# Optimization experiments

Hardware: AMD Instinct MI355X
Metric: run time of the kernel (lower is better)

## Reference

```python
import jax, jax.numpy as jnp
import numpy as np
import math

B, S, D, DFF = 32, 2048, 512, 512


def setup_inputs() -> dict:
    key = jax.random.key(0)
    ks = jax.random.split(key, 10)
    s = 1.0 / math.sqrt(D)
    inp = {
        "x": jax.random.normal(ks[0], (B, S, D), dtype=jnp.float32),
        "Wq": jax.random.uniform(ks[1], (DFF, D), jnp.float32, -s, s),
        "bq": jax.random.uniform(ks[2], (DFF,), jnp.float32, -s, s),
        "Wk": jax.random.uniform(ks[3], (DFF, D), jnp.float32, -s, s),
        "bk": jax.random.uniform(ks[4], (DFF,), jnp.float32, -s, s),
        "Wv": jax.random.uniform(ks[5], (DFF, D), jnp.float32, -s, s),
        "bv": jax.random.uniform(ks[6], (DFF,), jnp.float32, -s, s),
        "Wt": jax.random.uniform(ks[7], (1, S), jnp.float32, -1.0 / math.sqrt(S), 1.0 / math.sqrt(S)),
        "bt": jax.random.uniform(ks[8], (1,), jnp.float32, -1.0 / math.sqrt(S), 1.0 / math.sqrt(S)),
    }
    return inp


def reference(x, Wq, bq, Wk, bk, Wv, bv, Wt, bt):
    # QKV projections: [B,S,DFF]
    q = jnp.einsum('bsd,fd->bsf', x, Wq) + bq
    k = jnp.einsum('bsd,fd->bsf', x, Wk) + bk
    v = jnp.einsum('bsd,fd->bsf', x, Wv) + bv
    # attention scores: [B,S,S]
    scores = jnp.einsum('bsf,btf->bst', q, k) / math.sqrt(DFF)
    # temporal reduction Linear(S->1): [B,S,1] -> [B,S]
    ta = jnp.einsum('bst,t->bs', scores, Wt[0]) + bt[0]
    # V-weighted sum: [B,DFF]
    latent = jnp.einsum('bsf,bs->bf', v, ta)
    return latent
```

## Files before the change

### kernel.cpp

```cpp
#include <hip/hip_runtime.h>

#define NB 32
#define NS 2048
#define ND 512
#define NFF 512
#define SCALE 0.044194173824159216f

__device__ __forceinline__ float dot4(float4 a, float4 b) {
    return a.x * b.x + a.y * b.y + a.z * b.z + a.w * b.w;
}

__device__ __forceinline__ float wave_reduce(float p) {
#pragma unroll
    for (int m = 1; m < 64; m <<= 1) p += __shfl_xor(p, m, 64);
    return p;
}

__global__ void __launch_bounds__(256) k_xw(const float* __restrict__ x,
                                            const float* __restrict__ Wt,
                                            float* __restrict__ xwp) {
    const int b = blockIdx.x >> 5;
    const int chunk = blockIdx.x & 31;
    const int s0 = chunk * 64;
    const int t = threadIdx.x;
    const int col = t & 127;
    const int half = t >> 7;
    const float4* xb = (const float4*)(x + (size_t)b * NS * ND);
    float4 acc = make_float4(0.f, 0.f, 0.f, 0.f);
#pragma unroll 4
    for (int i = 0; i < 32; i++) {
        int s = s0 + half + 2 * i;
        float w = Wt[s];
        float4 v = xb[(size_t)s * 128 + col];
        acc.x += w * v.x; acc.y += w * v.y; acc.z += w * v.z; acc.w += w * v.w;
    }
    __shared__ float4 red[128];
    if (half == 1) red[col] = acc;
    __syncthreads();
    if (half == 0) {
        float4 o = red[col];
        o.x += acc.x; o.y += acc.y; o.z += acc.z; o.w += acc.w;
        ((float4*)xwp)[(size_t)blockIdx.x * 128 + col] = o;
    }
}

__global__ void __launch_bounds__(1024) k_kwq(const float* __restrict__ xwp,
                                              const float* __restrict__ Wt,
                                              const float* __restrict__ Wk,
                                              const float* __restrict__ bk,
                                              const float* __restrict__ Wq,
                                              const float* __restrict__ bq,
                                              const float* __restrict__ bt,
                                              float* __restrict__ wqs,
                                              float* __restrict__ cb2) {
    const int b = blockIdx.x;
    const int t = threadIdx.x;
    const int wv = t >> 6;
    const int lane = t & 63;
    __shared__ float xw[ND];
    __shared__ float kwl[NFF];
    __shared__ float part[2][ND];
    __shared__ float cbred[16];
    __shared__ float swt_s;

    if (t < ND) {
        float a = 0.f;
        const float* p = xwp + (size_t)b * 32 * ND + t;
#pragma unroll
        for (int c = 0; c < 32; c++) a += p[c * ND];
        xw[t] = a;
    }
    if (wv == 15) {
        float a = 0.f;
#pragma unroll
        for (int j = 0; j < 32; j++) a += Wt[j * 64 + lane];
        a = wave_reduce(a);
        if (lane == 0) swt_s = a;
    }
    __syncthreads();

    {
        const float4* xw4 = (const float4*)xw;
        const float4 xa = xw4[lane];
        const float4 xc = xw4[64 + lane];
        const float sw = swt_s;
        float cbp = 0.f;
#pragma unroll 4
        for (int j = 0; j < 32; j++) {
            int f = wv * 32 + j;
            const float4* wr = (const float4*)(Wk + (size_t)f * ND);
            float p = dot4(xa, wr[lane]) + dot4(xc, wr[64 + lane]);
            p = wave_reduce(p);
            if (lane == 0) {
                float kf = p + bk[f] * sw;
                kwl[f] = kf;
                cbp += kf * bq[f];
            }
        }
        if (lane == 0) cbred[wv] = cbp;
    }
    __syncthreads();

    {
        const int d = t & 511;
        const int h = t >> 9;
        float acc = 0.f;
        const int f0 = h * 256;
#pragma unroll 8
        for (int j = 0; j < 256; j++) {
            int f = f0 + j;
            acc += kwl[f] * Wq[(size_t)f * ND + d];
        }
        part[h][d] = acc;
        if (t == 0) {
            float s = 0.f;
#pragma unroll
            for (int w = 0; w < 16; w++) s += cbred[w];
            cb2[b] = SCALE * s + bt[0];
        }
    }
    __syncthreads();
    if (t < ND) wqs[b * ND + t] = SCALE * (part[0][t] + part[1][t]);
}

__global__ void __launch_bounds__(256) k_ta_xt(const float* __restrict__ x,
                                               const float* __restrict__ wqs,
                                               const float* __restrict__ cb2,
                                               float* __restrict__ xtp,
                                               float* __restrict__ stp) {
    const int b = blockIdx.x >> 5;
    const int chunk = blockIdx.x & 31;
    const int wave = threadIdx.x >> 6;
    const int lane = threadIdx.x & 63;
    const float4* xb = (const float4*)(x + (size_t)b * NS * ND);
    const float4* wq4 = (const float4*)(wqs + b * ND);
    const float4 w0 = wq4[lane];
    const float4 w1 = wq4[64 + lane];
    const float c = cb2[b];
    float4 a0 = make_float4(0.f, 0.f, 0.f, 0.f);
    float4 a1 = make_float4(0.f, 0.f, 0.f, 0.f);
    float sta = 0.f;
#pragma unroll 2
    for (int i = 0; i < 16; i++) {
        int s = chunk * 64 + wave * 16 + i;
        float4 v0 = xb[(size_t)s * 128 + lane];
        float4 v1 = xb[(size_t)s * 128 + 64 + lane];
        float p = dot4(v0, w0) + dot4(v1, w1);
        p = wave_reduce(p);
        float ta = p + c;
        a0.x += ta * v0.x; a0.y += ta * v0.y; a0.z += ta * v0.z; a0.w += ta * v0.w;
        a1.x += ta * v1.x; a1.y += ta * v1.y; a1.z += ta * v1.z; a1.w += ta * v1.w;
        sta += ta;
    }
    __shared__ float4 sh0[4][64];
    __shared__ float4 sh1[4][64];
    __shared__ float stw[4];
    sh0[wave][lane] = a0;
    sh1[wave][lane] = a1;
    if (lane == 0) stw[wave] = sta;
    __syncthreads();
    const int t = threadIdx.x;
    float4* dst = (float4*)xtp + (size_t)blockIdx.x * 128;
    if (t < 64) {
        float4 s0 = sh0[0][t], s1 = sh0[1][t], s2 = sh0[2][t], s3 = sh0[3][t];
        dst[t] = make_float4(s0.x + s1.x + s2.x + s3.x,
                             s0.y + s1.y + s2.y + s3.y,
                             s0.z + s1.z + s2.z + s3.z,
                             s0.w + s1.w + s2.w + s3.w);
    } else if (t < 128) {
        int l = t - 64;
        float4 s0 = sh1[0][l], s1 = sh1[1][l], s2 = sh1[2][l], s3 = sh1[3][l];
        dst[64 + l] = make_float4(s0.x + s1.x + s2.x + s3.x,
                                  s0.y + s1.y + s2.y + s3.y,
                                  s0.z + s1.z + s2.z + s3.z,
                                  s0.w + s1.w + s2.w + s3.w);
    } else if (t == 128) {
        stp[blockIdx.x] = stw[0] + stw[1] + stw[2] + stw[3];
    }
}

__global__ void __launch_bounds__(256) k_latent(const float* __restrict__ xtp,
                                                const float* __restrict__ stp,
                                                const float* __restrict__ Wv,
                                                const float* __restrict__ bv,
                                                float* __restrict__ out) {
    const int b = blockIdx.x >> 3;
    const int t = threadIdx.x;
    __shared__ float xt[ND];
    __shared__ float sts;
    {
        float a0 = 0.f, a1 = 0.f;
        const float* p = xtp + (size_t)b * 32 * ND;
#pragma unroll
        for (int c = 0; c < 32; c++) {
            a0 += p[c * ND + t];
            a1 += p[c * ND + 256 + t];
        }
        xt[t] = a0;
        xt[256 + t] = a1;
        if (t == 0) {
            float s = 0.f;
            const float* sp = stp + b * 32;
#pragma unroll
            for (int c = 0; c < 32; c++) s += sp[c];
            sts = s;
        }
    }
    __syncthreads();
    const int wv = t >> 6;
    const int lane = t & 63;
    const int f0 = ((blockIdx.x & 7) * 4 + wv) * 16;
    const float4* xt4 = (const float4*)xt;
    const float4 xa = xt4[lane];
    const float4 xc = xt4[64 + lane];
    const float stb = sts;
#pragma unroll 4
    for (int j = 0; j < 16; j++) {
        int f = f0 + j;
        const float4* wr = (const float4*)(Wv + (size_t)f * ND);
        float p = dot4(xa, wr[lane]) + dot4(xc, wr[64 + lane]);
        p = wave_reduce(p);
        if (lane == 0) out[b * NFF + f] = p + bv[f] * stb;
    }
}

extern "C" void kernel_launch(void* const* d_in, const int* in_sizes, int n_in,
                              void* d_out, int out_size, void* d_ws, size_t ws_size,
                              hipStream_t stream) {
    const float* x  = (const float*)d_in[0];
    const float* Wq = (const float*)d_in[1];
    const float* bq = (const float*)d_in[2];
    const float* Wk = (const float*)d_in[3];
    const float* bk = (const float*)d_in[4];
    const float* Wv = (const float*)d_in[5];
    const float* bv = (const float*)d_in[6];
    const float* Wt = (const float*)d_in[7];
    const float* bt = (const float*)d_in[8];
    float* out = (float*)d_out;

    float* w = (float*)d_ws;
    float* xwp = w;
    float* xtp = w + 524288;
    float* stp = w + 1048576;
    float* wqs = w + 1049600;
    float* cb2 = w + 1065984;

    k_xw<<<NB * 32, 256, 0, stream>>>(x, Wt, xwp);
    k_kwq<<<NB, 1024, 0, stream>>>(xwp, Wt, Wk, bk, Wq, bq, bt, wqs, cb2);
    k_ta_xt<<<NB * 32, 256, 0, stream>>>(x, wqs, cb2, xtp, stp);
    k_latent<<<256, 256, 0, stream>>>(xtp, stp, Wv, bv, out);
}
```

Baseline: 295.0 us.

## Fuse four kernels into one cooperative kernel with grid-wide syncs

Replaces the four separate launches (xw reduction, kw/wq projection, ta/xt pass, latent projection) with a single cooperative kernel of 512 blocks that separates the stages with grid.sync(). The kw/wq stage is spread over 256 and 128 blocks instead of 32 blocks of 1024 threads, and each block now handles 128 rows instead of 64. The aim is to cut launch gaps and the serial tail of the small 32-block middle kernel. The cost is grid-barrier overhead and idle blocks during the small stages, and x is still read twice from memory.

```diff
diff --git a/kernel.cpp b/kernel.cpp
--- a/kernel.cpp
+++ b/kernel.cpp
@@ -1,4 +1,7 @@
 #include <hip/hip_runtime.h>
+#include <hip/hip_cooperative_groups.h>
+
+namespace cg = cooperative_groups;
 
 #define NB 32
 #define NS 2048
@@ -6,6 +9,10 @@
 #define NFF 512
 #define SCALE 0.044194173824159216f
 
+#define NBLK 512
+#define CPB 16
+#define ROWS 128
+
 __device__ __forceinline__ float dot4(float4 a, float4 b) {
     return a.x * b.x + a.y * b.y + a.z * b.z + a.w * b.w;
 }
@@ -16,211 +23,204 @@
     return p;
 }
 
-__global__ void __launch_bounds__(256) k_xw(const float* __restrict__ x,
-                                            const float* __restrict__ Wt,
-                                            float* __restrict__ xwp) {
-    const int b = blockIdx.x >> 5;
-    const int chunk = blockIdx.x & 31;
-    const int s0 = chunk * 64;
-    const int t = threadIdx.x;
-    const int col = t & 127;
-    const int half = t >> 7;
-    const float4* xb = (const float4*)(x + (size_t)b * NS * ND);
-    float4 acc = make_float4(0.f, 0.f, 0.f, 0.f);
+__global__ void __launch_bounds__(256, 2)
+k_fused(const float* __restrict__ x,
+        const float* __restrict__ Wq, const float* __restrict__ bq,
+        const float* __restrict__ Wk, const float* __restrict__ bk,
+        const float* __restrict__ Wv, const float* __restrict__ bv,
+        const float* __restrict__ Wt, const float* __restrict__ bt,
+        float* __restrict__ out, float* __restrict__ ws) {
+    cg::grid_group grid = cg::this_grid();
+
+    float* xwp  = ws;
+    float* xtp  = ws + 262144;
+    float* stp  = ws + 524288;
+    float* kw   = ws + 524800;
+    float* wqs  = ws + 541184;
+    float* kwbq = ws + 557568;
+    float* cb2  = ws + 557824;
+
+    const int blk  = blockIdx.x;
+    const int t    = threadIdx.x;
+    const int wv   = t >> 6;
+    const int lane = t & 63;
+    const int b_s  = blk >> 4;
+    const int chunk = blk & 15;
+
+    __shared__ float4 red4[128];
+    __shared__ float4 sh0[4][64];
+    __shared__ float4 sh1[4][64];
+    __shared__ float  sA[ND];
+    __shared__ float  part[2][128];
+    __shared__ float  sW[4];
+    __shared__ float  sScalar;
+
+    const float4* xb = (const float4*)(x + (size_t)b_s * NS * ND);
+
+    {
+        const int col = t & 127;
+        const int half = t >> 7;
+        const int s0 = chunk * ROWS;
+        float4 acc = make_float4(0.f, 0.f, 0.f, 0.f);
 #pragma unroll 4
-    for (int i = 0; i < 32; i++) {
-        int s = s0 + half + 2 * i;
-        float w = Wt[s];
-        float4 v = xb[(size_t)s * 128 + col];
-        acc.x += w * v.x; acc.y += w * v.y; acc.z += w * v.z; acc.w += w * v.w;
-    }
-    __shared__ float4 red[128];
-    if (half == 1) red[col] = acc;
-    __syncthreads();
-    if (half == 0) {
-        float4 o = red[col];
-        o.x += acc.x; o.y += acc.y; o.z += acc.z; o.w += acc.w;
-        ((float4*)xwp)[(size_t)blockIdx.x * 128 + col] = o;
-    }
-}
-
-__global__ void __launch_bounds__(1024) k_kwq(const float* __restrict__ xwp,
-                                              const float* __restrict__ Wt,
-                                              const float* __restrict__ Wk,
-                                              const float* __restrict__ bk,
-                                              const float* __restrict__ Wq,
-                                              const float* __restrict__ bq,
-                                              const float* __restrict__ bt,
-                                              float* __restrict__ wqs,
-                                              float* __restrict__ cb2) {
-    const int b = blockIdx.x;
-    const int t = threadIdx.x;
-    const int wv = t >> 6;
-    const int lane = t & 63;
-    __shared__ float xw[ND];
-    __shared__ float kwl[NFF];
-    __shared__ float part[2][ND];
-    __shared__ float cbred[16];
-    __shared__ float swt_s;
-
-    if (t < ND) {
-        float a = 0.f;
-        const float* p = xwp + (size_t)b * 32 * ND + t;
-#pragma unroll
-        for (int c = 0; c < 32; c++) a += p[c * ND];
-        xw[t] = a;
-    }
-    if (wv == 15) {
-        float a = 0.f;
-#pragma unroll
-        for (int j = 0; j < 32; j++) a += Wt[j * 64 + lane];
-        a = wave_reduce(a);
-        if (lane == 0) swt_s = a;
-    }
-    __syncthreads();
-
-    {
-        const float4* xw4 = (const float4*)xw;
+        for (int i = 0; i < 64; i++) {
+            int s = s0 + half + 2 * i;
+            float w = Wt[s];
+            float4 v = xb[(size_t)s * 128 + col];
+            acc.x += w * v.x; acc.y += w * v.y; acc.z += w * v.z; acc.w += w * v.w;
+        }
+        if (half == 1) red4[col] = acc;
+        __syncthreads();
+        if (half == 0) {
+            float4 o = red4[col];
+            o.x += acc.x; o.y += acc.y; o.z += acc.z; o.w += acc.w;
+            ((float4*)xwp)[(size_t)blk * 128 + col] = o;
+        }
+    }
+    grid.sync();
+
+    if (blk < 256) {
+        const int b = blk >> 3;
+        const int f0 = (blk & 7) * 64;
+        float a0 = 0.f, a1 = 0.f;
+        const float* p = xwp + (size_t)b * CPB * ND;
+#pragma unroll
+        for (int c = 0; c < CPB; c++) {
+            a0 += p[c * ND + t];
+            a1 += p[c * ND + 256 + t];
+        }
+        sA[t] = a0;
+        sA[256 + t] = a1;
+        if (wv == 0) {
+            float a = 0.f;
+#pragma unroll
+            for (int j = 0; j < 32; j++) a += Wt[j * 64 + lane];
+            a = wave_reduce(a);
+            if (lane == 0) sScalar = a;
+        }
+        __syncthreads();
+        const float4* xw4 = (const float4*)sA;
         const float4 xa = xw4[lane];
         const float4 xc = xw4[64 + lane];
-        const float sw = swt_s;
+        const float sw = sScalar;
         float cbp = 0.f;
 #pragma unroll 4
-        for (int j = 0; j < 32; j++) {
-            int f = wv * 32 + j;
+        for (int j = 0; j < 16; j++) {
+            int f = f0 + wv * 16 + j;
             const float4* wr = (const float4*)(Wk + (size_t)f * ND);
-            float p = dot4(xa, wr[lane]) + dot4(xc, wr[64 + lane]);
-            p = wave_reduce(p);
+            float pd = dot4(xa, wr[lane]) + dot4(xc, wr[64 + lane]);
+            pd = wave_reduce(pd);
             if (lane == 0) {
-                float kf = p + bk[f] * sw;
-                kwl[f] = kf;
+                float kf = pd + bk[f] * sw;
+                kw[b * NFF + f] = kf;
                 cbp += kf * bq[f];
             }
         }
-        if (lane == 0) cbred[wv] = cbp;
-    }
-    __syncthreads();
+        if (lane == 0) sW[wv] = cbp;
+        __syncthreads();
+        if (t == 0) kwbq[blk] = sW[0] + sW[1] + sW[2] + sW[3];
+    }
+    grid.sync();
+
+    if (blk < 128) {
+        const int b = blk >> 2;
+        const int d0 = (blk & 3) * 128;
+        const int dl = t & 127;
+        const int h = t >> 7;
+        float acc = 0.f;
+        const float* kwb = kw + b * NFF + h * 256;
+        const float* wq = Wq + (size_t)h * 256 * ND + d0 + dl;
+#pragma unroll 8
+        for (int j = 0; j < 256; j++) acc += kwb[j] * wq[(size_t)j * ND];
+        part[h][dl] = acc;
+        __syncthreads();
+        if (h == 0) wqs[b * ND + d0 + dl] = SCALE * (part[0][dl] + part[1][dl]);
+        if ((blk & 3) == 0 && t == 0) {
+            float s = 0.f;
+#pragma unroll
+            for (int k = 0; k < 8; k++) s += kwbq[b * 8 + k];
+            cb2[b] = SCALE * s + bt[0];
+        }
+    }
+    grid.sync();
 
     {
-        const int d = t & 511;
-        const int h = t >> 9;
-        float acc = 0.f;
-        const int f0 = h * 256;
-#pragma unroll 8
-        for (int j = 0; j < 256; j++) {
-            int f = f0 + j;
-            acc += kwl[f] * Wq[(size_t)f * ND + d];
-        }
-        part[h][d] = acc;
+        const float4* wq4 = (const float4*)(wqs + b_s * ND);
+        const float4 w0 = wq4[lane];
+        const float4 w1 = wq4[64 + lane];
+        const float c = cb2[b_s];
+        float4 a0 = make_float4(0.f, 0.f, 0.f, 0.f);
+        float4 a1 = make_float4(0.f, 0.f, 0.f, 0.f);
+        float sta = 0.f;
+#pragma unroll 2
+        for (int i = 0; i < 32; i++) {
+            int s = chunk * ROWS + wv * 32 + i;
+            float4 v0 = xb[(size_t)s * 128 + lane];
+            float4 v1 = xb[(size_t)s * 128 + 64 + lane];
+            float pd = dot4(v0, w0) + dot4(v1, w1);
+            pd = wave_reduce(pd);
+            float ta = pd + c;
+            a0.x += ta * v0.x; a0.y += ta * v0.y; a0.z += ta * v0.z; a0.w += ta * v0.w;
+            a1.x += ta * v1.x; a1.y += ta * v1.y; a1.z += ta * v1.z; a1.w += ta * v1.w;
+            sta += ta;
+        }
+        __syncthreads();
+        sh0[wv][lane] = a0;
+        sh1[wv][lane] = a1;
+        if (lane == 0) sW[wv] = sta;
+        __syncthreads();
+        float4* dst = (float4*)xtp + (size_t)blk * 128;
+        if (t < 64) {
+            float4 s0 = sh0[0][t], s1 = sh0[1][t], s2 = sh0[2][t], s3 = sh0[3][t];
+            dst[t] = make_float4(s0.x + s1.x + s2.x + s3.x,
+                                 s0.y + s1.y + s2.y + s3.y,
+                                 s0.z + s1.z + s2.z + s3.z,
+                                 s0.w + s1.w + s2.w + s3.w);
+        } else if (t < 128) {
+            int l = t - 64;
+            float4 s0 = sh1[0][l], s1 = sh1[1][l], s2 = sh1[2][l], s3 = sh1[3][l];
+            dst[64 + l] = make_float4(s0.x + s1.x + s2.x + s3.x,
+                                      s0.y + s1.y + s2.y + s3.y,
+                                      s0.z + s1.z + s2.z + s3.z,
+                                      s0.w + s1.w + s2.w + s3.w);
+        } else if (t == 128) {
+            stp[blk] = sW[0] + sW[1] + sW[2] + sW[3];
+        }
+    }
+    grid.sync();
+
+    if (blk < 256) {
+        const int b = blk >> 3;
+        const int f0 = (blk & 7) * 64;
+        float a0 = 0.f, a1 = 0.f;
+        const float* p = xtp + (size_t)b * CPB * ND;
+#pragma unroll
+        for (int c = 0; c < CPB; c++) {
+            a0 += p[c * ND + t];
+            a1 += p[c * ND + 256 + t];
+        }
+        __syncthreads();
+        sA[t] = a0;
+        sA[256 + t] = a1;
         if (t == 0) {
             float s = 0.f;
 #pragma unroll
-            for (int w = 0; w < 16; w++) s += cbred[w];
-            cb2[b] = SCALE * s + bt[0];
-        }
-    }
-    __syncthreads();
-    if (t < ND) wqs[b * ND + t] = SCALE * (part[0][t] + part[1][t]);
-}
-
-__global__ void __launch_bounds__(256) k_ta_xt(const float* __restrict__ x,
-                                               const float* __restrict__ wqs,
-                                               const float* __restrict__ cb2,
-                                               float* __restrict__ xtp,
-                                               float* __restrict__ stp) {
-    const int b = blockIdx.x >> 5;
-    const int chunk = blockIdx.x & 31;
-    const int wave = threadIdx.x >> 6;
-    const int lane = threadIdx.x & 63;
-    const float4* xb = (const float4*)(x + (size_t)b * NS * ND);
-    const float4* wq4 = (const float4*)(wqs + b * ND);
-    const float4 w0 = wq4[lane];
-    const float4 w1 = wq4[64 + lane];
-    const float c = cb2[b];
-    float4 a0 = make_float4(0.f, 0.f, 0.f, 0.f);
-    float4 a1 = make_float4(0.f, 0.f, 0.f, 0.f);
-    float sta = 0.f;
-#pragma unroll 2
-    for (int i = 0; i < 16; i++) {
-        int s = chunk * 64 + wave * 16 + i;
-        float4 v0 = xb[(size_t)s * 128 + lane];
-        float4 v1 = xb[(size_t)s * 128 + 64 + lane];
-        float p = dot4(v0, w0) + dot4(v1, w1);
-        p = wave_reduce(p);
-        float ta = p + c;
-        a0.x += ta * v0.x; a0.y += ta * v0.y; a0.z += ta * v0.z; a0.w += ta * v0.w;
-        a1.x += ta * v1.x; a1.y += ta * v1.y; a1.z += ta * v1.z; a1.w += ta * v1.w;
-        sta += ta;
-    }
-    __shared__ float4 sh0[4][64];
-    __shared__ float4 sh1[4][64];
-    __shared__ float stw[4];
-    sh0[wave][lane] = a0;
-    sh1[wave][lane] = a1;
-    if (lane == 0) stw[wave] = sta;
-    __syncthreads();
-    const int t = threadIdx.x;
-    float4* dst = (float4*)xtp + (size_t)blockIdx.x * 128;
-    if (t < 64) {
-        float4 s0 = sh0[0][t], s1 = sh0[1][t], s2 = sh0[2][t], s3 = sh0[3][t];
-        dst[t] = make_float4(s0.x + s1.x + s2.x + s3.x,
-                             s0.y + s1.y + s2.y + s3.y,
-                             s0.z + s1.z + s2.z + s3.z,
-                             s0.w + s1.w + s2.w + s3.w);
-    } else if (t < 128) {
-        int l = t - 64;
-        float4 s0 = sh1[0][l], s1 = sh1[1][l], s2 = sh1[2][l], s3 = sh1[3][l];
-        dst[64 + l] = make_float4(s0.x + s1.x + s2.x + s3.x,
-                                  s0.y + s1.y + s2.y + s3.y,
-                                  s0.z + s1.z + s2.z + s3.z,
-                                  s0.w + s1.w + s2.w + s3.w);
-    } else if (t == 128) {
-        stp[blockIdx.x] = stw[0] + stw[1] + stw[2] + stw[3];
-    }
-}
-
-__global__ void __launch_bounds__(256) k_latent(const float* __restrict__ xtp,
-                                                const float* __restrict__ stp,
-                                                const float* __restrict__ Wv,
-                                                const float* __restrict__ bv,
-                                                float* __restrict__ out) {
-    const int b = blockIdx.x >> 3;
-    const int t = threadIdx.x;
-    __shared__ float xt[ND];
-    __shared__ float sts;
-    {
-        float a0 = 0.f, a1 = 0.f;
-        const float* p = xtp + (size_t)b * 32 * ND;
-#pragma unroll
-        for (int c = 0; c < 32; c++) {
-            a0 += p[c * ND + t];
-            a1 += p[c * ND + 256 + t];
-        }
-        xt[t] = a0;
-        xt[256 + t] = a1;
-        if (t == 0) {
-            float s = 0.f;
-            const float* sp = stp + b * 32;
-#pragma unroll
-            for (int c = 0; c < 32; c++) s += sp[c];
-            sts = s;
-        }
-    }
-    __syncthreads();
-    const int wv = t >> 6;
-    const int lane = t & 63;
-    const int f0 = ((blockIdx.x & 7) * 4 + wv) * 16;
-    const float4* xt4 = (const float4*)xt;
-    const float4 xa = xt4[lane];
-    const float4 xc = xt4[64 + lane];
-    const float stb = sts;
+            for (int c = 0; c < CPB; c++) s += stp[b * CPB + c];
+            sScalar = s;
+        }
+        __syncthreads();
+        const float4* xt4 = (const float4*)sA;
+        const float4 xa = xt4[lane];
+        const float4 xc = xt4[64 + lane];
+        const float stb = sScalar;
 #pragma unroll 4
-    for (int j = 0; j < 16; j++) {
-        int f = f0 + j;
-        const float4* wr = (const float4*)(Wv + (size_t)f * ND);
-        float p = dot4(xa, wr[lane]) + dot4(xc, wr[64 + lane]);
-        p = wave_reduce(p);
-        if (lane == 0) out[b * NFF + f] = p + bv[f] * stb;
+        for (int j = 0; j < 16; j++) {
+            int f = f0 + wv * 16 + j;
+            const float4* wr = (const float4*)(Wv + (size_t)f * ND);
+            float pd = dot4(xa, wr[lane]) + dot4(xc, wr[64 + lane]);
+            pd = wave_reduce(pd);
+            if (lane == 0) out[b * NFF + f] = pd + bv[f] * stb;
+        }
     }
 }
 
@@ -237,16 +237,10 @@
     const float* Wt = (const float*)d_in[7];
     const float* bt = (const float*)d_in[8];
     float* out = (float*)d_out;
-
-    float* w = (float*)d_ws;
-    float* xwp = w;
-    float* xtp = w + 524288;
-    float* stp = w + 1048576;
-    float* wqs = w + 1049600;
-    float* cb2 = w + 1065984;
-
-    k_xw<<<NB * 32, 256, 0, stream>>>(x, Wt, xwp);
-    k_kwq<<<NB, 1024, 0, stream>>>(xwp, Wt, Wk, bk, Wq, bq, bt, wqs, cb2);
-    k_ta_xt<<<NB * 32, 256, 0, stream>>>(x, wqs, cb2, xtp, stp);
-    k_latent<<<256, 256, 0, stream>>>(xtp, stp, Wv, bv, out);
-}
+    float* wsf = (float*)d_ws;
+
+    void* args[] = {(void*)&x, (void*)&Wq, (void*)&bq, (void*)&Wk, (void*)&bk,
+                    (void*)&Wv, (void*)&bv, (void*)&Wt, (void*)&bt,
+                    (void*)&out, (void*)&wsf};
+    hipLaunchCooperativeKernel((void*)k_fused, dim3(NBLK), dim3(256), args, 0, stream);
+}
```

After: 511.9 us. +73.5%, slower.

## Split key/query weight stage into wider kernels and double chunk count per batch

Applied to the files above, without the earlier changes.

The single 32-block, 1024-thread kernel that computed the Wk projection and the Wq back-projection is split into two kernels with 256 and 128 blocks. This spreads the small weight matvecs across more compute units instead of one block per batch. The x-streaming kernels now use 64 chunks of 32 rows per batch instead of 32 chunks of 64, doubling their grid to 2048 blocks for better occupancy. The cost is an extra launch, more partial sums written and reduced, and a larger workspace.

```diff
diff --git a/kernel.cpp b/kernel.cpp
--- a/kernel.cpp
+++ b/kernel.cpp
@@ -6,6 +6,9 @@
 #define NFF 512
 #define SCALE 0.044194173824159216f
 
+#define CPB 64
+#define ROWS 32
+
 __device__ __forceinline__ float dot4(float4 a, float4 b) {
     return a.x * b.x + a.y * b.y + a.z * b.z + a.w * b.w;
 }
@@ -19,16 +22,16 @@
 __global__ void __launch_bounds__(256) k_xw(const float* __restrict__ x,
                                             const float* __restrict__ Wt,
                                             float* __restrict__ xwp) {
-    const int b = blockIdx.x >> 5;
-    const int chunk = blockIdx.x & 31;
-    const int s0 = chunk * 64;
+    const int b = blockIdx.x >> 6;
+    const int chunk = blockIdx.x & 63;
+    const int s0 = chunk * ROWS;
     const int t = threadIdx.x;
     const int col = t & 127;
     const int half = t >> 7;
     const float4* xb = (const float4*)(x + (size_t)b * NS * ND);
     float4 acc = make_float4(0.f, 0.f, 0.f, 0.f);
 #pragma unroll 4
-    for (int i = 0; i < 32; i++) {
+    for (int i = 0; i < 16; i++) {
         int s = s0 + half + 2 * i;
         float w = Wt[s];
         float4 v = xb[(size_t)s * 128 + col];
@@ -44,33 +47,33 @@
     }
 }
 
-__global__ void __launch_bounds__(1024) k_kwq(const float* __restrict__ xwp,
-                                              const float* __restrict__ Wt,
-                                              const float* __restrict__ Wk,
-                                              const float* __restrict__ bk,
-                                              const float* __restrict__ Wq,
-                                              const float* __restrict__ bq,
-                                              const float* __restrict__ bt,
-                                              float* __restrict__ wqs,
-                                              float* __restrict__ cb2) {
-    const int b = blockIdx.x;
+__global__ void __launch_bounds__(256) k_kw(const float* __restrict__ xwp,
+                                            const float* __restrict__ Wt,
+                                            const float* __restrict__ Wk,
+                                            const float* __restrict__ bk,
+                                            const float* __restrict__ bq,
+                                            float* __restrict__ kw,
+                                            float* __restrict__ kwbq) {
+    const int b = blockIdx.x >> 3;
+    const int f0 = (blockIdx.x & 7) * 64;
     const int t = threadIdx.x;
     const int wv = t >> 6;
     const int lane = t & 63;
-    __shared__ float xw[ND];
-    __shared__ float kwl[NFF];
-    __shared__ float part[2][ND];
-    __shared__ float cbred[16];
+    __shared__ float sA[ND];
+    __shared__ float sW[4];
     __shared__ float swt_s;
-
-    if (t < ND) {
-        float a = 0.f;
-        const float* p = xwp + (size_t)b * 32 * ND + t;
-#pragma unroll
-        for (int c = 0; c < 32; c++) a += p[c * ND];
-        xw[t] = a;
-    }
-    if (wv == 15) {
+    {
+        float a0 = 0.f, a1 = 0.f;
+        const float* p = xwp + (size_t)b * CPB * ND + t;
+#pragma unroll 8
+        for (int c = 0; c < CPB; c++) {
+            a0 += p[(size_t)c * ND];
+            a1 += p[(size_t)c * ND + 256];
+        }
+        sA[t] = a0;
+        sA[256 + t] = a1;
+    }
+    if (wv == 0) {
         float a = 0.f;
 #pragma unroll
         for (int j = 0; j < 32; j++) a += Wt[j * 64 + lane];
@@ -78,49 +81,54 @@
         if (lane == 0) swt_s = a;
     }
     __syncthreads();
-
-    {
-        const float4* xw4 = (const float4*)xw;
-        const float4 xa = xw4[lane];
-        const float4 xc = xw4[64 + lane];
-        const float sw = swt_s;
-        float cbp = 0.f;
+    const float4* xw4 = (const float4*)sA;
+    const float4 xa = xw4[lane];
+    const float4 xc = xw4[64 + lane];
+    const float sw = swt_s;
+    float cbp = 0.f;
 #pragma unroll 4
-        for (int j = 0; j < 32; j++) {
-            int f = wv * 32 + j;
-            const float4* wr = (const float4*)(Wk + (size_t)f * ND);
-            float p = dot4(xa, wr[lane]) + dot4(xc, wr[64 + lane]);
-            p = wave_reduce(p);
-            if (lane == 0) {
-                float kf = p + bk[f] * sw;
-                kwl[f] = kf;
-                cbp += kf * bq[f];
-            }
-        }
-        if (lane == 0) cbred[wv] = cbp;
-    }
-    __syncthreads();
-
-    {
-        const int d = t & 511;
-        const int h = t >> 9;
-        float acc = 0.f;
-        const int f0 = h * 256;
+    for (int j = 0; j < 16; j++) {
+        int f = f0 + wv * 16 + j;
+        const float4* wr = (const float4*)(Wk + (size_t)f * ND);
+        float pd = dot4(xa, wr[lane]) + dot4(xc, wr[64 + lane]);
+        pd = wave_reduce(pd);
+        if (lane == 0) {
+            float kf = pd + bk[f] * sw;
+            kw[b * NFF + f] = kf;
+            cbp += kf * bq[f];
+        }
+    }
+    if (lane == 0) sW[wv] = cbp;
+    __syncthreads();
+    if (t == 0) kwbq[blockIdx.x] = sW[0] + sW[1] + sW[2] + sW[3];
+}
+
+__global__ void __launch_bounds__(256) k_wqs(const float* __restrict__ kw,
+                                             const float* __restrict__ Wq,
+                                             const float* __restrict__ kwbq,
+                                             const float* __restrict__ bt,
+                                             float* __restrict__ wqs,
+                                             float* __restrict__ cb2) {
+    const int b = blockIdx.x >> 2;
+    const int d0 = (blockIdx.x & 3) * 128;
+    const int t = threadIdx.x;
+    const int dl = t & 127;
+    const int h = t >> 7;
+    __shared__ float part[2][128];
+    float acc = 0.f;
+    const float* kwb = kw + b * NFF + h * 256;
+    const float* wq = Wq + (size_t)h * 256 * ND + d0 + dl;
 #pragma unroll 8
-        for (int j = 0; j < 256; j++) {
-            int f = f0 + j;
-            acc += kwl[f] * Wq[(size_t)f * ND + d];
-        }
-        part[h][d] = acc;
-        if (t == 0) {
-            float s = 0.f;
-#pragma unroll
-            for (int w = 0; w < 16; w++) s += cbred[w];
-            cb2[b] = SCALE * s + bt[0];
-        }
-    }
-    __syncthreads();
-    if (t < ND) wqs[b * ND + t] = SCALE * (part[0][t] + part[1][t]);
+    for (int j = 0; j < 256; j++) acc += kwb[j] * wq[(size_t)j * ND];
+    part[h][dl] = acc;
+    __syncthreads();
+    if (h == 0) wqs[b * ND + d0 + dl] = SCALE * (part[0][dl] + part[1][dl]);
+    if ((blockIdx.x & 3) == 0 && t == 0) {
+        float s = 0.f;
+#pragma unroll
+        for (int k = 0; k < 8; k++) s += kwbq[b * 8 + k];
+        cb2[b] = SCALE * s + bt[0];
+    }
 }
 
 __global__ void __launch_bounds__(256) k_ta_xt(const float* __restrict__ x,
@@ -128,9 +136,9 @@
                                                const float* __restrict__ cb2,
                                                float* __restrict__ xtp,
                                                float* __restrict__ stp) {
-    const int b = blockIdx.x >> 5;
-    const int chunk = blockIdx.x & 31;
-    const int wave = threadIdx.x >> 6;
+    const int b = blockIdx.x >> 6;
+    const int chunk = blockIdx.x & 63;
+    const int wv = threadIdx.x >> 6;
     const int lane = threadIdx.x & 63;
     const float4* xb = (const float4*)(x + (size_t)b * NS * ND);
     const float4* wq4 = (const float4*)(wqs + b * ND);
@@ -141,23 +149,23 @@
     float4 a1 = make_float4(0.f, 0.f, 0.f, 0.f);
     float sta = 0.f;
 #pragma unroll 2
-    for (int i = 0; i < 16; i++) {
-        int s = chunk * 64 + wave * 16 + i;
+    for (int i = 0; i < 8; i++) {
+        int s = chunk * ROWS + wv * 8 + i;
         float4 v0 = xb[(size_t)s * 128 + lane];
         float4 v1 = xb[(size_t)s * 128 + 64 + lane];
-        float p = dot4(v0, w0) + dot4(v1, w1);
-        p = wave_reduce(p);
-        float ta = p + c;
+        float pd = dot4(v0, w0) + dot4(v1, w1);
+        pd = wave_reduce(pd);
+        float ta = pd + c;
         a0.x += ta * v0.x; a0.y += ta * v0.y; a0.z += ta * v0.z; a0.w += ta * v0.w;
         a1.x += ta * v1.x; a1.y += ta * v1.y; a1.z += ta * v1.z; a1.w += ta * v1.w;
         sta += ta;
     }
     __shared__ float4 sh0[4][64];
     __shared__ float4 sh1[4][64];
-    __shared__ float stw[4];
-    sh0[wave][lane] = a0;
-    sh1[wave][lane] = a1;
-    if (lane == 0) stw[wave] = sta;
+    __shared__ float sW[4];
+    sh0[wv][lane] = a0;
+    sh1[wv][lane] = a1;
+    if (lane == 0) sW[wv] = sta;
     __syncthreads();
     const int t = threadIdx.x;
     float4* dst = (float4*)xtp + (size_t)blockIdx.x * 128;
@@ -175,7 +183,7 @@
                                   s0.z + s1.z + s2.z + s3.z,
                                   s0.w + s1.w + s2.w + s3.w);
     } else if (t == 128) {
-        stp[blockIdx.x] = stw[0] + stw[1] + stw[2] + stw[3];
+        stp[blockIdx.x] = sW[0] + sW[1] + sW[2] + sW[3];
     }
 }
 
@@ -185,42 +193,42 @@
                                                 const float* __restrict__ bv,
                                                 float* __restrict__ out) {
     const int b = blockIdx.x >> 3;
-    const int t = threadIdx.x;
-    __shared__ float xt[ND];
+    const int f0 = (blockIdx.x & 7) * 64;
+    const int t = threadIdx.x;
+    const int wv = t >> 6;
+    const int lane = t & 63;
+    __shared__ float sA[ND];
     __shared__ float sts;
     {
         float a0 = 0.f, a1 = 0.f;
-        const float* p = xtp + (size_t)b * 32 * ND;
-#pragma unroll
-        for (int c = 0; c < 32; c++) {
-            a0 += p[c * ND + t];
-            a1 += p[c * ND + 256 + t];
-        }
-        xt[t] = a0;
-        xt[256 + t] = a1;
+        const float* p = xtp + (size_t)b * CPB * ND + t;
+#pragma unroll 8
+        for (int c = 0; c < CPB; c++) {
+            a0 += p[(size_t)c * ND];
+            a1 += p[(size_t)c * ND + 256];
+        }
+        sA[t] = a0;
+        sA[256 + t] = a1;
         if (t == 0) {
             float s = 0.f;
-            const float* sp = stp + b * 32;
-#pragma unroll
-            for (int c = 0; c < 32; c++) s += sp[c];
+            const float* sp = stp + b * CPB;
+#pragma unroll
+            for (int c = 0; c < CPB; c++) s += sp[c];
             sts = s;
         }
     }
     __syncthreads();
-    const int wv = t >> 6;
-    const int lane = t & 63;
-    const int f0 = ((blockIdx.x & 7) * 4 + wv) * 16;
-    const float4* xt4 = (const float4*)xt;
+    const float4* xt4 = (const float4*)sA;
     const float4 xa = xt4[lane];
     const float4 xc = xt4[64 + lane];
     const float stb = sts;
 #pragma unroll 4
     for (int j = 0; j < 16; j++) {
-        int f = f0 + j;
+        int f = f0 + wv * 16 + j;
         const float4* wr = (const float4*)(Wv + (size_t)f * ND);
-        float p = dot4(xa, wr[lane]) + dot4(xc, wr[64 + lane]);
-        p = wave_reduce(p);
-        if (lane == 0) out[b * NFF + f] = p + bv[f] * stb;
+        float pd = dot4(xa, wr[lane]) + dot4(xc, wr[64 + lane]);
+        pd = wave_reduce(pd);
+        if (lane == 0) out[b * NFF + f] = pd + bv[f] * stb;
     }
 }
 
@@ -239,14 +247,17 @@
     float* out = (float*)d_out;
 
     float* w = (float*)d_ws;
-    float* xwp = w;
-    float* xtp = w + 524288;
-    float* stp = w + 1048576;
-    float* wqs = w + 1049600;
-    float* cb2 = w + 1065984;
-
-    k_xw<<<NB * 32, 256, 0, stream>>>(x, Wt, xwp);
-    k_kwq<<<NB, 1024, 0, stream>>>(xwp, Wt, Wk, bk, Wq, bq, bt, wqs, cb2);
-    k_ta_xt<<<NB * 32, 256, 0, stream>>>(x, wqs, cb2, xtp, stp);
+    float* xwp  = w;
+    float* xtp  = w + 1048576;
+    float* stp  = w + 2097152;
+    float* kw   = w + 2099200;
+    float* kwbq = w + 2115584;
+    float* wqs  = w + 2115840;
+    float* cb2  = w + 2132224;
+
+    k_xw<<<NB * CPB, 256, 0, stream>>>(x, Wt, xwp);
+    k_kw<<<256, 256, 0, stream>>>(xwp, Wt, Wk, bk, bq, kw, kwbq);
+    k_wqs<<<128, 256, 0, stream>>>(kw, Wq, kwbq, bt, wqs, cb2);
+    k_ta_xt<<<NB * CPB, 256, 0, stream>>>(x, wqs, cb2, xtp, stp);
     k_latent<<<256, 256, 0, stream>>>(xtp, stp, Wv, bv, out);
 }
```

After: 280.7 us. -4.8%, faster.
